# Kernel optimization log

Hardware: AMD Instinct MI355X
Metric: run time of the kernel (lower is better)

Reference implementation:

```python
import jax, jax.numpy as jnp
import numpy as np


def setup_inputs() -> dict:
    key = jax.random.key(0)
    ks = jax.random.split(key, 8)
    N, E, F_IN, H, OUT = 20000, 320000, 386, 256, 2
    x = jax.random.normal(ks[0], (N, F_IN), dtype=jnp.float32)
    src = jax.random.randint(ks[1], (E,), 0, N)
    dst = jax.random.randint(ks[2], (E,), 0, N)
    W1 = jax.random.normal(ks[3], (F_IN, H), dtype=jnp.float32) / np.sqrt(F_IN)
    b1 = jnp.zeros((H,), dtype=jnp.float32)
    W2 = jax.random.normal(ks[4], (H, OUT), dtype=jnp.float32) / np.sqrt(H)
    b2 = jnp.zeros((OUT,), dtype=jnp.float32)
    return {"x": x, "src": src, "dst": dst, "W1": W1, "b1": b1, "W2": W2, "b2": b2}


def reference(x, src, dst, W1, b1, W2, b2):
    N = x.shape[0]
    # PyG GCNConv: add self-loops, deg from destination (col), sym normalization
    deg = jnp.ones((N,), x.dtype).at[dst].add(1.0)  # self-loop + in-degree
    dis = deg ** -0.5                                # deg^{-1/2}
    edge_norm = dis[src] * dis[dst]                  # [E]
    self_norm = dis * dis                            # [N] (self-loop weight)

    def gcn_conv(h, W, b):
        h = h @ W                                    # [N, F_out] transform first
        msgs = h[src] * edge_norm[:, None]           # [E, F_out] gathered messages
        agg = jax.ops.segment_sum(msgs, dst, num_segments=N)
        agg = agg + h * self_norm[:, None]           # self-loop contribution
        return agg + b

    h = jax.nn.relu(gcn_conv(x, W1, b1))
    out = gcn_conv(h, W2, b2)
    return jnp.tanh(out)
```

## Files before the change

kernel.cpp:

```cpp
#include <hip/hip_runtime.h>
#include <math.h>

typedef _Float16 f16;
typedef _Float16 f16x8 __attribute__((ext_vector_type(8)));
typedef float f32x4 __attribute__((ext_vector_type(4)));

#define FIN 386
#define KP  416
#define HH  256
#define ELLW 64
#define NP  20032

#define BTM 64
#define BTN 64
#define GBK 32


__global__ __launch_bounds__(256) void k_prep(
    int* __restrict__ cursor, int N,
    const float* __restrict__ W1, f16* __restrict__ wt,
    const float* __restrict__ x, f16* __restrict__ xh) {
    int i = blockIdx.x * 256 + threadIdx.x;
    if (i < N) cursor[i] = 0;
    if (i < HH * KP) {
        int c = i / KP, k = i - c * KP;
        wt[i] = (k < FIN) ? (f16)W1[(size_t)k * HH + c] : (f16)0.f;
    }
    const int CPR = KP / 8;
    if (i < NP * CPR) {
        int row = i / CPR;
        int k2 = (i - row * CPR) * 8;
        f16x8 t = {};
        if (row < N && k2 < FIN) {
            const float* p = x + (size_t)row * FIN + k2;
            if (k2 + 8 <= FIN) {
                float2 f0 = *(const float2*)(p);
                float2 f1 = *(const float2*)(p + 2);
                float2 f2 = *(const float2*)(p + 4);
                float2 f3 = *(const float2*)(p + 6);
                t[0] = (f16)f0.x; t[1] = (f16)f0.y;
                t[2] = (f16)f1.x; t[3] = (f16)f1.y;
                t[4] = (f16)f2.x; t[5] = (f16)f2.y;
                t[6] = (f16)f3.x; t[7] = (f16)f3.y;
            } else {
                #pragma unroll
                for (int j = 0; j < 8; ++j)
                    t[j] = (k2 + j < FIN) ? (f16)p[j] : (f16)0.f;
            }
        }
        *(f16x8*)(xh + (size_t)row * KP + k2) = t;
    }
}


__global__ __launch_bounds__(256, 5) void k_mid(
    const f16* __restrict__ A, const f16* __restrict__ Bt,
    f16* __restrict__ C, int nbg,
    const int* __restrict__ src, const int* __restrict__ dst,
    int* __restrict__ cursor, int* __restrict__ ell, int E, int nbf) {

    if ((int)blockIdx.x >= nbg) {
        for (int e = ((int)blockIdx.x - nbg) * 256 + threadIdx.x; e < E; e += nbf * 256) {
            int s = src[e], d = dst[e];
            int slot = atomicAdd(&cursor[d], 1);
            if (slot < ELLW) ell[(size_t)d * ELLW + slot] = s;
        }
        return;
    }

    const int gb = blockIdx.x;
    const int bm = (gb >> 2) * BTM;
    const int bn = (gb & 3) * BTN;
    const int tid = threadIdx.x;
    const int w = tid >> 6, l = tid & 63;
    const int lrow = l & 15, lslot = l >> 4;

    const f16* pa = A  + (size_t)(bm + w * 16 + lrow) * KP + lslot * 8;
    const f16* pb = Bt + (size_t)(bn + lrow) * KP + lslot * 8;

    f32x4 acc[4] = {};

    #pragma unroll
    for (int k0 = 0; k0 < KP; k0 += GBK) {
        f16x8 a  = *(const f16x8*)(pa + k0);
        f16x8 b0 = *(const f16x8*)(pb + k0);
        f16x8 b1 = *(const f16x8*)(pb + (size_t)16 * KP + k0);
        f16x8 b2 = *(const f16x8*)(pb + (size_t)32 * KP + k0);
        f16x8 b3 = *(const f16x8*)(pb + (size_t)48 * KP + k0);
        acc[0] = __builtin_amdgcn_mfma_f32_16x16x32_f16(a, b0, acc[0], 0, 0, 0);
        acc[1] = __builtin_amdgcn_mfma_f32_16x16x32_f16(a, b1, acc[1], 0, 0, 0);
        acc[2] = __builtin_amdgcn_mfma_f32_16x16x32_f16(a, b2, acc[2], 0, 0, 0);
        acc[3] = __builtin_amdgcn_mfma_f32_16x16x32_f16(a, b3, acc[3], 0, 0, 0);
    }

    #pragma unroll
    for (int r = 0; r < 4; ++r) {
        int row = bm + w * 16 + lslot * 4 + r;
        #pragma unroll
        for (int ni = 0; ni < 4; ++ni)
            C[(size_t)row * HH + bn + ni * 16 + lrow] = (f16)acc[ni][r];
    }
}


__global__ __launch_bounds__(256) void k_agg1(
    const f16* __restrict__ h1h, const int* __restrict__ ell,
    const int* __restrict__ cursor, const float* __restrict__ b1,
    const float* __restrict__ W2, float* __restrict__ z, int N) {
    const int sl = threadIdx.x & 31;
    const int d = blockIdx.x * 8 + (threadIdx.x >> 5);
    if (d >= N) return;

    const float4* bp = (const float4*)b1 + sl * 2;
    const float4 bb0 = bp[0], bb1 = bp[1];
    const float4* wp = (const float4*)W2 + sl * 4;
    const float4 wv0 = wp[0], wv1 = wp[1], wv2 = wp[2], wv3 = wp[3];

    int cd = cursor[d];
    float dd = rsqrtf((float)(cd + 1));
    int cnt = cd > ELLW ? ELLW : cd;
    const int* erow = ell + (size_t)d * ELLW;

    f16x8 v = ((const f16x8*)(h1h + (size_t)d * HH))[sl];
    float e[8];
    #pragma unroll
    for (int i = 0; i < 8; ++i) e[i] = dd * (float)v[i];

    int j = 0;
    for (; j + 3 < cnt; j += 4) {
        int s0 = erow[j], s1 = erow[j + 1], s2 = erow[j + 2], s3 = erow[j + 3];
        float u0 = rsqrtf((float)(cursor[s0] + 1));
        float u1 = rsqrtf((float)(cursor[s1] + 1));
        float u2 = rsqrtf((float)(cursor[s2] + 1));
        float u3 = rsqrtf((float)(cursor[s3] + 1));
        f16x8 q0 = ((const f16x8*)(h1h + (size_t)s0 * HH))[sl];
        f16x8 q1 = ((const f16x8*)(h1h + (size_t)s1 * HH))[sl];
        f16x8 q2 = ((const f16x8*)(h1h + (size_t)s2 * HH))[sl];
        f16x8 q3 = ((const f16x8*)(h1h + (size_t)s3 * HH))[sl];
        #pragma unroll
        for (int i = 0; i < 8; ++i)
            e[i] += u0 * (float)q0[i] + u1 * (float)q1[i]
                  + u2 * (float)q2[i] + u3 * (float)q3[i];
    }
    for (; j < cnt; ++j) {
        int s0 = erow[j];
        float u0 = rsqrtf((float)(cursor[s0] + 1));
        f16x8 q0 = ((const f16x8*)(h1h + (size_t)s0 * HH))[sl];
        #pragma unroll
        for (int i = 0; i < 8; ++i) e[i] += u0 * (float)q0[i];
    }

    float a[8];
    a[0] = fmaxf(dd * e[0] + bb0.x, 0.0f);
    a[1] = fmaxf(dd * e[1] + bb0.y, 0.0f);
    a[2] = fmaxf(dd * e[2] + bb0.z, 0.0f);
    a[3] = fmaxf(dd * e[3] + bb0.w, 0.0f);
    a[4] = fmaxf(dd * e[4] + bb1.x, 0.0f);
    a[5] = fmaxf(dd * e[5] + bb1.y, 0.0f);
    a[6] = fmaxf(dd * e[6] + bb1.z, 0.0f);
    a[7] = fmaxf(dd * e[7] + bb1.w, 0.0f);

    float p0 = a[0] * wv0.x + a[1] * wv0.z + a[2] * wv1.x + a[3] * wv1.z
             + a[4] * wv2.x + a[5] * wv2.z + a[6] * wv3.x + a[7] * wv3.z;
    float p1 = a[0] * wv0.y + a[1] * wv0.w + a[2] * wv1.y + a[3] * wv1.w
             + a[4] * wv2.y + a[5] * wv2.w + a[6] * wv3.y + a[7] * wv3.w;
    #pragma unroll
    for (int off = 16; off > 0; off >>= 1) {
        p0 += __shfl_down(p0, off, 32);
        p1 += __shfl_down(p1, off, 32);
    }
    if (sl == 0)
        *(float2*)(z + 2 * (size_t)d) = make_float2(p0, p1);
}


__global__ __launch_bounds__(256) void k_agg2(
    const float* __restrict__ z, const int* __restrict__ ell,
    const int* __restrict__ cursor, const float* __restrict__ b2,
    float* __restrict__ out, int N) {
    int d = blockIdx.x * 256 + threadIdx.x;
    if (d >= N) return;
    const float c0 = b2[0], c1 = b2[1];
    int cd = cursor[d];
    float dd = rsqrtf((float)(cd + 1));
    int cnt = cd > ELLW ? ELLW : cd;
    const int* erow = ell + (size_t)d * ELLW;
    float2 zz = *(const float2*)(z + 2 * (size_t)d);
    float e0 = dd * zz.x, e1 = dd * zz.y;
    int j = 0;
    for (; j + 3 < cnt; j += 4) {
        int s0 = erow[j], s1 = erow[j + 1], s2 = erow[j + 2], s3 = erow[j + 3];
        float u0 = rsqrtf((float)(cursor[s0] + 1));
        float u1 = rsqrtf((float)(cursor[s1] + 1));
        float u2 = rsqrtf((float)(cursor[s2] + 1));
        float u3 = rsqrtf((float)(cursor[s3] + 1));
        float2 z0 = *(const float2*)(z + 2 * (size_t)s0);
        float2 z1 = *(const float2*)(z + 2 * (size_t)s1);
        float2 z2 = *(const float2*)(z + 2 * (size_t)s2);
        float2 z3 = *(const float2*)(z + 2 * (size_t)s3);
        e0 += u0 * z0.x + u1 * z1.x + u2 * z2.x + u3 * z3.x;
        e1 += u0 * z0.y + u1 * z1.y + u2 * z2.y + u3 * z3.y;
    }
    for (; j < cnt; ++j) {
        int s = erow[j];
        float u = rsqrtf((float)(cursor[s] + 1));
        float2 zv = *(const float2*)(z + 2 * (size_t)s);
        e0 += u * zv.x;
        e1 += u * zv.y;
    }
    out[d * 2 + 0] = tanhf(dd * e0 + c0);
    out[d * 2 + 1] = tanhf(dd * e1 + c1);
}


extern "C" void kernel_launch(void* const* d_in, const int* in_sizes, int n_in,
                              void* d_out, int out_size, void* d_ws, size_t ws_size,
                              hipStream_t stream) {
    const float* x   = (const float*)d_in[0];
    const int*   src = (const int*)d_in[1];
    const int*   dst = (const int*)d_in[2];
    const float* W1  = (const float*)d_in[3];
    const float* b1  = (const float*)d_in[4];
    const float* W2  = (const float*)d_in[5];
    const float* b2  = (const float*)d_in[6];
    float* out = (float*)d_out;

    const int E = in_sizes[1];
    const int N = in_sizes[0] / FIN;

    char* base = (char*)d_ws;
    size_t off = 0;
    f16* wt     = (f16*)(base + off); off += (size_t)HH * KP * sizeof(f16);
    f16* xh     = (f16*)(base + off); off += (size_t)NP * KP * sizeof(f16);
    f16* h1h    = (f16*)(base + off); off += (size_t)NP * HH * sizeof(f16);
    int* ell    = (int*)(base + off); off += (size_t)N * ELLW * sizeof(int);
    float* z    = (float*)(base + off); off += 2 * (size_t)N * sizeof(float);
    int* cursor = (int*)(base + off); off += (size_t)N * sizeof(int);

    const int T = 256;
    const int CPR = KP / 8;
    const int prep_work = NP * CPR;
    const int nbg = (NP / BTM) * (HH / BTN);
    const int nbf = 512;

    k_prep<<<(prep_work + T - 1) / T, T, 0, stream>>>(cursor, N, W1, wt, x, xh);
    k_mid<<<nbg + nbf, T, 0, stream>>>(xh, wt, h1h, nbg, src, dst, cursor, ell, E, nbf);
    k_agg1<<<(N + 7) / 8, T, 0, stream>>>(h1h, ell, cursor, b1, W2, z, N);
    k_agg2<<<(N + T - 1) / T, T, 0, stream>>>(z, ell, cursor, b2, out, N);
}
```

Measured before the change: 81.32 us.

## Stage B tile in LDS, double M tile per block, prefetch A fragments

The GEMM block now copies the whole 64xKP slice of the transposed weight into shared memory once and reads B fragments from LDS, instead of each wave reloading B from global memory. Each wave computes two 16-row M fragments (BTM 128), so every B fragment feeds two MFMAs, and the next A fragments are prefetched one k-step ahead. The padded row count is raised to match the larger M tile. The cost is about 53 KB of LDS per block and more registers, and the occupancy hint of 5 blocks is dropped. Fewer GEMM blocks also changes how the GEMM and ELL-fill blocks share the grid.

```diff
diff --git a/kernel.cpp b/kernel.cpp
--- a/kernel.cpp
+++ b/kernel.cpp
@@ -9,9 +9,9 @@
 #define KP  416
 #define HH  256
 #define ELLW 64
-#define NP  20032
-
-#define BTM 64
+#define NP  20096
+
+#define BTM 128
 #define BTN 64
 #define GBK 32
 
@@ -53,11 +53,12 @@
 }
 
 
-__global__ __launch_bounds__(256, 5) void k_mid(
+__global__ __launch_bounds__(256) void k_mid(
     const f16* __restrict__ A, const f16* __restrict__ Bt,
     f16* __restrict__ C, int nbg,
     const int* __restrict__ src, const int* __restrict__ dst,
     int* __restrict__ cursor, int* __restrict__ ell, int E, int nbf) {
+    __shared__ f16 Bs[BTN * KP];
 
     if ((int)blockIdx.x >= nbg) {
         for (int e = ((int)blockIdx.x - nbg) * 256 + threadIdx.x; e < E; e += nbf * 256) {
@@ -75,30 +76,46 @@
     const int w = tid >> 6, l = tid & 63;
     const int lrow = l & 15, lslot = l >> 4;
 
-    const f16* pa = A  + (size_t)(bm + w * 16 + lrow) * KP + lslot * 8;
-    const f16* pb = Bt + (size_t)(bn + lrow) * KP + lslot * 8;
-
-    f32x4 acc[4] = {};
+    for (int c = tid; c < BTN * (KP / 8); c += 256) {
+        int row = c / (KP / 8);
+        int k8 = (c - row * (KP / 8)) * 8;
+        *(f16x8*)&Bs[row * KP + k8] = *(const f16x8*)(Bt + (size_t)(bn + row) * KP + k8);
+    }
+    __syncthreads();
+
+    const f16* pa0 = A + (size_t)(bm + w * 32 + lrow) * KP + lslot * 8;
+    const f16* pa1 = pa0 + (size_t)16 * KP;
+
+    f32x4 acc[2][4] = {};
+
+    f16x8 a0c = *(const f16x8*)(pa0);
+    f16x8 a1c = *(const f16x8*)(pa1);
 
     #pragma unroll
     for (int k0 = 0; k0 < KP; k0 += GBK) {
-        f16x8 a  = *(const f16x8*)(pa + k0);
-        f16x8 b0 = *(const f16x8*)(pb + k0);
-        f16x8 b1 = *(const f16x8*)(pb + (size_t)16 * KP + k0);
-        f16x8 b2 = *(const f16x8*)(pb + (size_t)32 * KP + k0);
-        f16x8 b3 = *(const f16x8*)(pb + (size_t)48 * KP + k0);
-        acc[0] = __builtin_amdgcn_mfma_f32_16x16x32_f16(a, b0, acc[0], 0, 0, 0);
-        acc[1] = __builtin_amdgcn_mfma_f32_16x16x32_f16(a, b1, acc[1], 0, 0, 0);
-        acc[2] = __builtin_amdgcn_mfma_f32_16x16x32_f16(a, b2, acc[2], 0, 0, 0);
-        acc[3] = __builtin_amdgcn_mfma_f32_16x16x32_f16(a, b3, acc[3], 0, 0, 0);
-    }
-
-    #pragma unroll
-    for (int r = 0; r < 4; ++r) {
-        int row = bm + w * 16 + lslot * 4 + r;
-        #pragma unroll
-        for (int ni = 0; ni < 4; ++ni)
-            C[(size_t)row * HH + bn + ni * 16 + lrow] = (f16)acc[ni][r];
+        f16x8 a0n = a0c, a1n = a1c;
+        if (k0 + GBK < KP) {
+            a0n = *(const f16x8*)(pa0 + k0 + GBK);
+            a1n = *(const f16x8*)(pa1 + k0 + GBK);
+        }
+        #pragma unroll
+        for (int ni = 0; ni < 4; ++ni) {
+            f16x8 b = *(const f16x8*)&Bs[(ni * 16 + lrow) * KP + lslot * 8 + k0];
+            acc[0][ni] = __builtin_amdgcn_mfma_f32_16x16x32_f16(a0c, b, acc[0][ni], 0, 0, 0);
+            acc[1][ni] = __builtin_amdgcn_mfma_f32_16x16x32_f16(a1c, b, acc[1][ni], 0, 0, 0);
+        }
+        a0c = a0n; a1c = a1n;
+    }
+
+    #pragma unroll
+    for (int mi = 0; mi < 2; ++mi) {
+        #pragma unroll
+        for (int r = 0; r < 4; ++r) {
+            int row = bm + w * 32 + mi * 16 + lslot * 4 + r;
+            #pragma unroll
+            for (int ni = 0; ni < 4; ++ni)
+                C[(size_t)row * HH + bn + ni * 16 + lrow] = (f16)acc[mi][ni][r];
+        }
     }
 }
 
```

Measured after the change: 72.17 us. 11.2% less time.
